# Kernel tuning notes

Hardware: AMD Instinct MI355X
Metric: run time of the kernel (lower is better)

Reference implementation:

```python
import jax, jax.numpy as jnp
import numpy as np

B, D, H, E, K = 16384, 4096, 2048, 64, 2
TEMPERATURE = 0.8  # training=True


def setup_inputs() -> dict:
    key = jax.random.key(0)
    k1, k2, k3 = jax.random.split(key, 3)
    x = jax.random.normal(k1, (B, D), dtype=jnp.float32)
    W1 = jax.random.normal(k2, (H, D), dtype=jnp.float32) * 0.02
    b1 = jnp.zeros((H,), dtype=jnp.float32)
    W2 = jax.random.normal(k3, (E, H), dtype=jnp.float32) * 0.02
    b2 = jnp.zeros((E,), dtype=jnp.float32)
    return {"x": x, "W1": W1, "b1": b1, "W2": W2, "b2": b2}


def reference(x, W1, b1, W2, b2):
    # router MLP: Linear(D->H) -> ReLU -> Linear(H->E)
    h = jax.nn.relu(jnp.einsum('bd,hd->bh', x, W1) + b1)
    router_logits = jnp.einsum('bh,eh->be', h, W2) + b2  # [B, E]

    # temperature-scaled softmax for routing
    routing_probs = jax.nn.softmax(router_logits / TEMPERATURE, axis=1)
    routing_weights, expert_indices = jax.lax.top_k(routing_probs, K)  # [B, K]
    routing_weights = routing_weights / routing_weights.sum(axis=1, keepdims=True)

    # entropy-based uncertainty uses UN-scaled logits
    full_probs = jax.nn.softmax(router_logits, axis=1)
    entropy = -jnp.sum(full_probs * jnp.log(full_probs + 1e-10), axis=1).mean()
    uncertainty = entropy / jnp.log(jnp.float32(E))
    return routing_weights, expert_indices, uncertainty
```

## Files before the change

### kernel.cpp

```cpp
#include <hip/hip_runtime.h>
#include <hip/hip_bf16.h>
#include <math.h>

#define B_ROWS 16384
#define D_DIM  4096
#define H_DIM  2048
#define E_DIM  64
#define TEMP   0.8f

typedef __bf16 bf16x8 __attribute__((ext_vector_type(8)));
typedef float  f32x4  __attribute__((ext_vector_type(4)));
typedef unsigned short ushort8 __attribute__((ext_vector_type(8)));

__device__ __forceinline__ unsigned short bf_rne(float f) {
  unsigned u = __float_as_uint(f);
  u += 0x7FFF + ((u >> 16) & 1);
  return (unsigned short)(u >> 16);
}

__device__ __forceinline__ void async_copy16(const void* g, void* l) {
  __builtin_amdgcn_global_load_lds(
      (const __attribute__((address_space(1))) void*)g,
      (__attribute__((address_space(3))) void*)l, 16, 0, 0);
}

__global__ __launch_bounds__(256) void split_kernel(
    const float* __restrict__ in, unsigned short* __restrict__ hi,
    unsigned short* __restrict__ lo) {
  const size_t i = ((size_t)blockIdx.x * 256 + threadIdx.x) * 8;
  float4 v0 = *(const float4*)(in + i);
  float4 v1 = *(const float4*)(in + i + 4);
  float f[8] = {v0.x, v0.y, v0.z, v0.w, v1.x, v1.y, v1.z, v1.w};
  ushort8 hv, lv;
#pragma unroll
  for (int j = 0; j < 8; ++j) {
    unsigned short h = bf_rne(f[j]);
    float fh = __uint_as_float(((unsigned)h) << 16);
    hv[j] = h;
    lv[j] = bf_rne(f[j] - fh);
  }
  *(ushort8*)(hi + i) = hv;
  *(ushort8*)(lo + i) = lv;
}

#define G_BM 256
#define G_BN 256
#define G_BK 32
#define G_NT (D_DIM / G_BK)

#define MFMA_TRIPLE(MIv, NIv, FAH, FAL, FBH, FBL)                               \
  _Pragma("unroll")                                                             \
  for (int mf = 0; mf < 4; ++mf) {                                              \
    _Pragma("unroll")                                                           \
    for (int nf = 0; nf < 2; ++nf) {                                            \
      f32x4 a = acc[MIv][mf][NIv][nf];                                          \
      a = __builtin_amdgcn_mfma_f32_16x16x32_bf16(FAH[mf], FBH[nf], a, 0, 0, 0);\
      a = __builtin_amdgcn_mfma_f32_16x16x32_bf16(FAL[mf], FBH[nf], a, 0, 0, 0);\
      a = __builtin_amdgcn_mfma_f32_16x16x32_bf16(FAH[mf], FBL[nf], a, 0, 0, 0);\
      acc[MIv][mf][NIv][nf] = a;                                                \
    }                                                                           \
  }

__global__ __launch_bounds__(512, 2) void gemm1_8ph_kernel(
    const unsigned short* __restrict__ xh, const unsigned short* __restrict__ xl,
    const unsigned short* __restrict__ w1h, const unsigned short* __restrict__ w1l,
    const float* __restrict__ b1,
    const unsigned short* __restrict__ w2h, const unsigned short* __restrict__ w2l,
    float* __restrict__ logitsP) {
  __shared__ unsigned short SMEM[65536];
  unsigned short* const LAh = SMEM;
  unsigned short* const LAl = SMEM + 16384;
  unsigned short* const LBh = SMEM + 32768;
  unsigned short* const LBl = SMEM + 49152;

  const int t    = threadIdx.x;
  const int lane = t & 63;
  const int w    = t >> 6;
  const int wm   = w >> 2;
  const int wn   = w & 3;

  const int wg   = blockIdx.x;
  const int xcd  = wg & 7;
  const int slot = wg >> 3;
  const int mt   = xcd * 8 + (slot >> 3);
  const int nt   = slot & 7;
  const int m0   = mt * G_BM;
  const int n0   = nt * G_BN;

  const int sr  = t >> 2;
  const int sc  = (t & 3) * 8;
  const int scs = sc ^ (((sr >> 1) & 3) << 3);
  const int t8  = t * 8;
  const unsigned short* gAh = xh  + (size_t)(m0 + sr) * D_DIM + scs;
  const unsigned short* gAl = xl  + (size_t)(m0 + sr) * D_DIM + scs;
  const unsigned short* gBh = w1h + (size_t)(n0 + sr) * D_DIM + scs;
  const unsigned short* gBl = w1l + (size_t)(n0 + sr) * D_DIM + scs;

  auto stageA = [&](int buf, int half, int kt) {
    const size_t go = (size_t)half * 128 * D_DIM + (size_t)kt * G_BK;
    const int lo = buf * 8192 + half * 4096 + t8;
    async_copy16(gAh + go, &LAh[lo]);
    async_copy16(gAl + go, &LAl[lo]);
  };
  auto stageB = [&](int buf, int half, int kt) {
    const size_t go = (size_t)half * 128 * D_DIM + (size_t)kt * G_BK;
    const int lo = buf * 8192 + half * 4096 + t8;
    async_copy16(gBh + go, &LBh[lo]);
    async_copy16(gBl + go, &LBl[lo]);
  };

  constexpr int SST[8] = {0,1,0,1,0,1,0,1};
  constexpr int SHF[8] = {1,1,0,0,1,1,0,0};
  constexpr int SBF[8] = {1,1,0,0,0,0,1,1};
  constexpr int STL[8] = {1,1,2,2,2,2,3,3};

  auto stagePhase = [&](int p, int i) {
    int tl = 2 * i + STL[p];
    if (tl > G_NT - 1) tl = G_NT - 1;
    if (SST[p] == 0) stageA(SBF[p], SHF[p], tl);
    else             stageB(SBF[p], SHF[p], tl);
  };

  const int fr = lane & 15;
  const int ko = (lane >> 4) * 8;
  const int fc = ko ^ (((fr >> 1) & 3) << 3);
  const int aO = (wm * 64 + fr) * 32 + fc;
  const int bO = (wn * 32 + fr) * 32 + fc;

  f32x4 acc[2][4][2][2];
#pragma unroll
  for (int a = 0; a < 2; ++a)
#pragma unroll
    for (int b = 0; b < 4; ++b)
#pragma unroll
      for (int c = 0; c < 2; ++c)
#pragma unroll
        for (int d = 0; d < 2; ++d) acc[a][b][c][d] = (f32x4)0.f;

  stageA(0, 0, 0); stageB(0, 0, 0);
  stageA(0, 1, 0); stageB(0, 1, 0);
  stageA(1, 0, 1); stageB(1, 0, 1);
  asm volatile("s_waitcnt vmcnt(4)" ::: "memory");
  __builtin_amdgcn_s_barrier();
  __builtin_amdgcn_sched_barrier(0);

  for (int i = 0; i < G_NT / 2; ++i) {
#pragma unroll
    for (int half = 0; half < 2; ++half) {
      const int base = half * 4;
      const int cb   = half * 8192;

      bf16x8 fah[4], fal[4];
      bf16x8 fbh0[2], fbl0[2];
      bf16x8 fbh1[2], fbl1[2];

#pragma unroll
      for (int mf = 0; mf < 4; ++mf) {
        fah[mf] = *(const bf16x8*)&LAh[cb + aO + mf * 512];
        fal[mf] = *(const bf16x8*)&LAl[cb + aO + mf * 512];
      }
#pragma unroll
      for (int nf = 0; nf < 2; ++nf) {
        fbh0[nf] = *(const bf16x8*)&LBh[cb + bO + nf * 512];
        fbl0[nf] = *(const bf16x8*)&LBl[cb + bO + nf * 512];
      }
      stagePhase(base + 0, i);
      __builtin_amdgcn_s_barrier();
      __builtin_amdgcn_sched_barrier(0);
      __builtin_amdgcn_s_setprio(1);
      MFMA_TRIPLE(0, 0, fah, fal, fbh0, fbl0)
      __builtin_amdgcn_s_setprio(0);
      __builtin_amdgcn_s_barrier();
      __builtin_amdgcn_sched_barrier(0);

#pragma unroll
      for (int nf = 0; nf < 2; ++nf) {
        fbh1[nf] = *(const bf16x8*)&LBh[cb + 4096 + bO + nf * 512];
        fbl1[nf] = *(const bf16x8*)&LBl[cb + 4096 + bO + nf * 512];
      }
      stagePhase(base + 1, i);
      __builtin_amdgcn_s_barrier();
      __builtin_amdgcn_sched_barrier(0);
      __builtin_amdgcn_s_setprio(1);
      MFMA_TRIPLE(0, 1, fah, fal, fbh1, fbl1)
      __builtin_amdgcn_s_setprio(0);
      __builtin_amdgcn_s_barrier();
      __builtin_amdgcn_sched_barrier(0);

#pragma unroll
      for (int mf = 0; mf < 4; ++mf) {
        fah[mf] = *(const bf16x8*)&LAh[cb + 4096 + aO + mf * 512];
        fal[mf] = *(const bf16x8*)&LAl[cb + 4096 + aO + mf * 512];
      }
      stagePhase(base + 2, i);
      __builtin_amdgcn_s_barrier();
      __builtin_amdgcn_sched_barrier(0);
      __builtin_amdgcn_s_setprio(1);
      MFMA_TRIPLE(1, 0, fah, fal, fbh0, fbl0)
      __builtin_amdgcn_s_setprio(0);
      __builtin_amdgcn_s_barrier();
      __builtin_amdgcn_sched_barrier(0);

      stagePhase(base + 3, i);
      __builtin_amdgcn_s_barrier();
      __builtin_amdgcn_sched_barrier(0);
      __builtin_amdgcn_s_setprio(1);
      MFMA_TRIPLE(1, 1, fah, fal, fbh1, fbl1)
      __builtin_amdgcn_s_setprio(0);
      asm volatile("s_waitcnt vmcnt(4)" ::: "memory");
      __builtin_amdgcn_s_barrier();
      __builtin_amdgcn_sched_barrier(0);
    }
  }
  asm volatile("s_waitcnt vmcnt(0)" ::: "memory");
  __syncthreads();

  unsigned short* const Hh = SMEM;
  unsigned short* const Hl = SMEM + 32768;

#pragma unroll
  for (int mi = 0; mi < 2; ++mi) {
#pragma unroll
    for (int ni = 0; ni < 2; ++ni)
#pragma unroll
      for (int nf = 0; nf < 2; ++nf) {
        const int colb = wn * 32 + ni * 128 + nf * 16 + fr;
        const float bias = b1[n0 + colb];
        const int u = colb >> 3, j = colb & 7;
#pragma unroll
        for (int mf = 0; mf < 4; ++mf) {
          const int rowb = wm * 64 + mf * 16 + (lane >> 4) * 4;
#pragma unroll
          for (int r = 0; r < 4; ++r) {
            const int rr = rowb + r;
            const float vv = fmaxf(acc[mi][mf][ni][nf][r] + bias, 0.f);
            const unsigned short hv = bf_rne(vv);
            const float fh = __uint_as_float(((unsigned)hv) << 16);
            const unsigned short lv = bf_rne(vv - fh);
            const int a = rr * 256 + ((u ^ (rr & 7)) << 3) + j;
            Hh[a] = hv;
            Hl[a] = lv;
          }
        }
      }
    __syncthreads();

    f32x4 lac[4];
#pragma unroll
    for (int nf = 0; nf < 4; ++nf) lac[nf] = (f32x4)0.f;

    const int arow = w * 16 + fr;
#pragma unroll
    for (int kf = 0; kf < 8; ++kf) {
      const int au = (kf * 4 + (lane >> 4)) ^ (arow & 7);
      bf16x8 ahi = *(const bf16x8*)&Hh[arow * 256 + au * 8];
      bf16x8 alo = *(const bf16x8*)&Hl[arow * 256 + au * 8];
#pragma unroll
      for (int nf = 0; nf < 4; ++nf) {
        const size_t boff = (size_t)(nf * 16 + fr) * H_DIM + n0 + kf * 32 + ko;
        bf16x8 bhi = *(const bf16x8*)(w2h + boff);
        bf16x8 blo = *(const bf16x8*)(w2l + boff);
        lac[nf] = __builtin_amdgcn_mfma_f32_16x16x32_bf16(ahi, bhi, lac[nf], 0, 0, 0);
        lac[nf] = __builtin_amdgcn_mfma_f32_16x16x32_bf16(alo, bhi, lac[nf], 0, 0, 0);
        lac[nf] = __builtin_amdgcn_mfma_f32_16x16x32_bf16(ahi, blo, lac[nf], 0, 0, 0);
      }
    }

    float* lpb = logitsP + (size_t)nt * ((size_t)B_ROWS * E_DIM);
#pragma unroll
    for (int nf = 0; nf < 4; ++nf) {
      const int e = nf * 16 + fr;
#pragma unroll
      for (int r = 0; r < 4; ++r) {
        const int grow = m0 + mi * 128 + w * 16 + (lane >> 4) * 4 + r;
        lpb[(size_t)grow * E_DIM + e] = lac[nf][r];
      }
    }
    __syncthreads();
  }
}

__global__ __launch_bounds__(256) void router_kernel(
    const float* __restrict__ lp, const float* __restrict__ b2,
    float* __restrict__ out, float* __restrict__ accum) {
  const int t = threadIdx.x;
  const size_t row = (size_t)blockIdx.x * 256 + t;
  const size_t PS = (size_t)B_ROWS * E_DIM;

  float lg[64];
#pragma unroll
  for (int e4 = 0; e4 < 16; ++e4) {
    float4 v = *(const float4*)(lp + row * E_DIM + e4 * 4);
    lg[e4 * 4 + 0] = v.x; lg[e4 * 4 + 1] = v.y;
    lg[e4 * 4 + 2] = v.z; lg[e4 * 4 + 3] = v.w;
  }
#pragma unroll
  for (int p = 1; p < 8; ++p) {
#pragma unroll
    for (int e4 = 0; e4 < 16; ++e4) {
      float4 v = *(const float4*)(lp + (size_t)p * PS + row * E_DIM + e4 * 4);
      lg[e4 * 4 + 0] += v.x; lg[e4 * 4 + 1] += v.y;
      lg[e4 * 4 + 2] += v.z; lg[e4 * 4 + 3] += v.w;
    }
  }
#pragma unroll
  for (int e = 0; e < E_DIM; ++e) lg[e] += b2[e];

  float l0 = lg[0]; int i0 = 0;
  float l1 = -INFINITY; int i1 = -1;
#pragma unroll
  for (int e = 1; e < E_DIM; ++e) {
    float v = lg[e];
    if (v > l0)      { l1 = l0; i1 = i0; l0 = v; i0 = e; }
    else if (v > l1) { l1 = v; i1 = e; }
  }

  const float eT = expf((l1 - l0) / TEMP);
  const float w0 = 1.f / (1.f + eT);
  const float w1 = eT / (1.f + eT);

  float Z = 0.f;
#pragma unroll
  for (int e = 0; e < E_DIM; ++e) Z += expf(lg[e] - l0);
  const float invZ = 1.f / Z;
  float ent = 0.f;
#pragma unroll
  for (int e = 0; e < E_DIM; ++e) {
    float p = expf(lg[e] - l0) * invZ;
    ent -= p * logf(p + 1e-10f);
  }

  out[row * 2 + 0] = w0;
  out[row * 2 + 1] = w1;
  out[(size_t)B_ROWS * 2 + row * 2 + 0] = (float)i0;
  out[(size_t)B_ROWS * 2 + row * 2 + 1] = (float)i1;

#pragma unroll
  for (int off = 32; off > 0; off >>= 1) ent += __shfl_down(ent, off);
  if ((t & 63) == 0) atomicAdd(accum, ent);
}

#define BM 128
#define BN 128
#define BKK 32

__global__ __launch_bounds__(256) void gemm1_fb_kernel(
    const float* __restrict__ x,
    const unsigned short* __restrict__ w1h,
    const unsigned short* __restrict__ w1l,
    const float* __restrict__ b1,
    unsigned short* __restrict__ hhp, unsigned short* __restrict__ hlp) {
  __shared__ unsigned short Ah[BM * BKK];
  __shared__ unsigned short Al[BM * BKK];
  __shared__ unsigned short Bh[BN * BKK];
  __shared__ unsigned short Bl[BN * BKK];

  const int t    = threadIdx.x;
  const int lane = t & 63;
  const int w    = t >> 6;
  const int wm   = w >> 1;
  const int wn   = w & 1;
  const int m0   = blockIdx.y * BM;
  const int n0   = blockIdx.x * BN;

  const int e0 = (w * 2 + 0) * 512 + lane * 8;
  const int e1 = (w * 2 + 1) * 512 + lane * 8;
  const int r0 = e0 >> 5, c0 = e0 & 31;
  const int r1 = e1 >> 5, c1 = e1 & 31;
  const unsigned short* bh_g0 = w1h + (size_t)(n0 + r0) * D_DIM + c0;
  const unsigned short* bh_g1 = w1h + (size_t)(n0 + r1) * D_DIM + c1;
  const unsigned short* bl_g0 = w1l + (size_t)(n0 + r0) * D_DIM + c0;
  const unsigned short* bl_g1 = w1l + (size_t)(n0 + r1) * D_DIM + c1;
  unsigned short* bh_l0 = &Bh[e0];
  unsigned short* bh_l1 = &Bh[e1];
  unsigned short* bl_l0 = &Bl[e0];
  unsigned short* bl_l1 = &Bl[e1];

  const int ar = t >> 1;
  const int ac = (t & 1) * 16;
  const float* xp = x + (size_t)(m0 + ar) * D_DIM + ac;
  unsigned short* ah_w = &Ah[ar * BKK + ac];
  unsigned short* al_w = &Al[ar * BKK + ac];

  const int koff = (lane >> 4) * 8;
  const unsigned short* a_rd[4];
  const unsigned short* b_rd[4];
#pragma unroll
  for (int f = 0; f < 4; ++f) {
    a_rd[f] = &Ah[(wm * 64 + f * 16 + (lane & 15)) * BKK + koff];
    b_rd[f] = &Bh[(wn * 64 + f * 16 + (lane & 15)) * BKK + koff];
  }
  const int lo_off_a = (int)(Al - Ah);
  const int lo_off_b = (int)(Bl - Bh);

  f32x4 acc[4][4];
#pragma unroll
  for (int i = 0; i < 4; ++i)
#pragma unroll
    for (int j = 0; j < 4; ++j) acc[i][j] = (f32x4)0.f;

  for (int k0 = 0; k0 < D_DIM; k0 += BKK) {
    async_copy16(bh_g0 + k0, bh_l0);
    async_copy16(bh_g1 + k0, bh_l1);
    async_copy16(bl_g0 + k0, bl_l0);
    async_copy16(bl_g1 + k0, bl_l1);

    float4 v[4];
#pragma unroll
    for (int j = 0; j < 4; ++j) v[j] = *(const float4*)(xp + k0 + j * 4);
    float f[16] = {v[0].x, v[0].y, v[0].z, v[0].w, v[1].x, v[1].y, v[1].z, v[1].w,
                   v[2].x, v[2].y, v[2].z, v[2].w, v[3].x, v[3].y, v[3].z, v[3].w};
    ushort8 hv0, hv1, lv0, lv1;
#pragma unroll
    for (int j = 0; j < 8; ++j) {
      unsigned short h = bf_rne(f[j]);
      float fh = __uint_as_float(((unsigned)h) << 16);
      hv0[j] = h;
      lv0[j] = bf_rne(f[j] - fh);
    }
#pragma unroll
    for (int j = 0; j < 8; ++j) {
      unsigned short h = bf_rne(f[8 + j]);
      float fh = __uint_as_float(((unsigned)h) << 16);
      hv1[j] = h;
      lv1[j] = bf_rne(f[8 + j] - fh);
    }
    *(ushort8*)(ah_w)     = hv0;
    *(ushort8*)(ah_w + 8) = hv1;
    *(ushort8*)(al_w)     = lv0;
    *(ushort8*)(al_w + 8) = lv1;

    __syncthreads();

    bf16x8 fa_h[4], fa_l[4], fb_h[4], fb_l[4];
#pragma unroll
    for (int ff = 0; ff < 4; ++ff) {
      fa_h[ff] = *(const bf16x8*)(a_rd[ff]);
      fa_l[ff] = *(const bf16x8*)(a_rd[ff] + lo_off_a);
      fb_h[ff] = *(const bf16x8*)(b_rd[ff]);
      fb_l[ff] = *(const bf16x8*)(b_rd[ff] + lo_off_b);
    }
#pragma unroll
    for (int i = 0; i < 4; ++i)
#pragma unroll
      for (int j = 0; j < 4; ++j) {
        acc[i][j] = __builtin_amdgcn_mfma_f32_16x16x32_bf16(fa_h[i], fb_h[j], acc[i][j], 0, 0, 0);
        acc[i][j] = __builtin_amdgcn_mfma_f32_16x16x32_bf16(fa_l[i], fb_h[j], acc[i][j], 0, 0, 0);
        acc[i][j] = __builtin_amdgcn_mfma_f32_16x16x32_bf16(fa_h[i], fb_l[j], acc[i][j], 0, 0, 0);
      }
    __syncthreads();
  }

#pragma unroll
  for (int fn = 0; fn < 4; ++fn) {
    const int n = n0 + wn * 64 + fn * 16 + (lane & 15);
    const float bias = b1[n];
#pragma unroll
    for (int fm = 0; fm < 4; ++fm) {
      const int mbase = m0 + wm * 64 + fm * 16 + (lane >> 4) * 4;
#pragma unroll
      for (int r = 0; r < 4; ++r) {
        const float vv = fmaxf(acc[fm][fn][r] + bias, 0.f);
        const unsigned short hv = bf_rne(vv);
        const float fh = __uint_as_float(((unsigned)hv) << 16);
        const unsigned short lv = bf_rne(vv - fh);
        hhp[(size_t)(mbase + r) * H_DIM + n] = hv;
        hlp[(size_t)(mbase + r) * H_DIM + n] = lv;
      }
    }
  }
}

#define F_BM 64
#define F_BK 64
#define F_NT (H_DIM / F_BK)

__global__ __launch_bounds__(256) void gemm2_router_kernel(
    const unsigned short* __restrict__ hhp,
    const unsigned short* __restrict__ hlp,
    const unsigned short* __restrict__ w2h,
    const unsigned short* __restrict__ w2l,
    const float* __restrict__ b2,
    float* __restrict__ out, float* __restrict__ accum) {
  __shared__ unsigned short Ahs[2 * 4096];
  __shared__ unsigned short Als[2 * 4096];
  __shared__ unsigned short Bhs[2 * 4096];
  __shared__ unsigned short Bls[2 * 4096];
  __shared__ float LG[F_BM][E_DIM + 1];

  const int t    = threadIdx.x;
  const int lane = t & 63;
  const int w    = t >> 6;
  const int m0   = blockIdx.x * F_BM;

  const int srow = w * 8 + (lane >> 3);
  const int scol = ((lane & 7) * 8) ^ (((lane >> 3) & 7) << 3);
  const int t8   = t * 8;
  const unsigned short* gAh = hhp + (size_t)(m0 + srow) * H_DIM + scol;
  const unsigned short* gAl = hlp + (size_t)(m0 + srow) * H_DIM + scol;
  const unsigned short* gBh = w2h + (size_t)srow * H_DIM + scol;
  const unsigned short* gBl = w2l + (size_t)srow * H_DIM + scol;

  auto stage2 = [&](int buf, int kt) {
    const size_t k0 = (size_t)kt * F_BK;
#pragma unroll
    for (int c = 0; c < 2; ++c) {
      const size_t go = k0 + (size_t)c * 32 * H_DIM;
      const int lo = buf * 4096 + c * 2048 + t8;
      async_copy16(gAh + go, &Ahs[lo]);
      async_copy16(gAl + go, &Als[lo]);
      async_copy16(gBh + go, &Bhs[lo]);
      async_copy16(gBl + go, &Bls[lo]);
    }
  };

  const int fr = lane & 15;
  const int ko = (lane >> 4) * 8;
  const int Ra = w * 16 + fr;
  int aoff[2], boff[2][4];
#pragma unroll
  for (int kk = 0; kk < 2; ++kk) {
    aoff[kk] = Ra * 64 + ((kk * 32 + ko) ^ ((Ra & 7) << 3));
#pragma unroll
    for (int f = 0; f < 4; ++f) {
      const int Rb = f * 16 + fr;
      boff[kk][f] = Rb * 64 + ((kk * 32 + ko) ^ ((Rb & 7) << 3));
    }
  }

  f32x4 acc[4];
#pragma unroll
  for (int f = 0; f < 4; ++f) acc[f] = (f32x4)0.f;

  stage2(0, 0);
  int buf = 0;
  for (int kt = 0; kt < F_NT; ++kt) {
    if (kt + 1 < F_NT) {
      stage2(buf ^ 1, kt + 1);
      asm volatile("s_waitcnt vmcnt(8)" ::: "memory");
    } else {
      asm volatile("s_waitcnt vmcnt(0)" ::: "memory");
    }
    __builtin_amdgcn_s_barrier();
    __builtin_amdgcn_sched_barrier(0);
    const int bo = buf * 4096;
#pragma unroll
    for (int kk = 0; kk < 2; ++kk) {
      bf16x8 fa_h = *(const bf16x8*)&Ahs[bo + aoff[kk]];
      bf16x8 fa_l = *(const bf16x8*)&Als[bo + aoff[kk]];
#pragma unroll
      for (int f = 0; f < 4; ++f) {
        bf16x8 fb_h = *(const bf16x8*)&Bhs[bo + boff[kk][f]];
        bf16x8 fb_l = *(const bf16x8*)&Bls[bo + boff[kk][f]];
        acc[f] = __builtin_amdgcn_mfma_f32_16x16x32_bf16(fa_h, fb_h, acc[f], 0, 0, 0);
        acc[f] = __builtin_amdgcn_mfma_f32_16x16x32_bf16(fa_l, fb_h, acc[f], 0, 0, 0);
        acc[f] = __builtin_amdgcn_mfma_f32_16x16x32_bf16(fa_h, fb_l, acc[f], 0, 0, 0);
      }
    }
    __builtin_amdgcn_s_barrier();
    __builtin_amdgcn_sched_barrier(0);
    buf ^= 1;
  }

#pragma unroll
  for (int f = 0; f < 4; ++f) {
    const int e = f * 16 + fr;
    const float bias = b2[e];
#pragma unroll
    for (int r = 0; r < 4; ++r) {
      const int ml = w * 16 + (lane >> 4) * 4 + r;
      LG[ml][e] = acc[f][r] + bias;
    }
  }
  __syncthreads();

  if (t < F_BM) {
    const int row = m0 + t;
    float l0 = LG[t][0]; int i0 = 0;
    float l1 = -INFINITY; int i1 = -1;
#pragma unroll
    for (int e = 1; e < E_DIM; ++e) {
      float v = LG[t][e];
      if (v > l0)      { l1 = l0; i1 = i0; l0 = v; i0 = e; }
      else if (v > l1) { l1 = v; i1 = e; }
    }

    const float eT = expf((l1 - l0) / TEMP);
    const float w0 = 1.f / (1.f + eT);
    const float w1 = eT / (1.f + eT);

    float Z = 0.f;
#pragma unroll
    for (int e = 0; e < E_DIM; ++e) Z += expf(LG[t][e] - l0);
    const float invZ = 1.f / Z;
    float ent = 0.f;
#pragma unroll
    for (int e = 0; e < E_DIM; ++e) {
      float p = expf(LG[t][e] - l0) * invZ;
      ent -= p * logf(p + 1e-10f);
    }

    out[(size_t)row * 2 + 0] = w0;
    out[(size_t)row * 2 + 1] = w1;
    out[(size_t)B_ROWS * 2 + (size_t)row * 2 + 0] = (float)i0;
    out[(size_t)B_ROWS * 2 + (size_t)row * 2 + 1] = (float)i1;

#pragma unroll
    for (int off = 32; off > 0; off >>= 1) ent += __shfl_down(ent, off);
    if (t == 0) atomicAdd(accum, ent);
  }
}

__global__ void zero_kernel(float* p) { p[0] = 0.f; }

__global__ void finalize_kernel(const float* __restrict__ accum,
                                float* __restrict__ out) {
  out[(size_t)B_ROWS * 4] = accum[0] / ((float)B_ROWS * logf((float)E_DIM));
}

extern "C" void kernel_launch(void* const* d_in, const int* in_sizes, int n_in,
                              void* d_out, int out_size, void* d_ws,
                              size_t ws_size, hipStream_t stream) {
  const float* x  = (const float*)d_in[0];
  const float* W1 = (const float*)d_in[1];
  const float* b1 = (const float*)d_in[2];
  const float* W2 = (const float*)d_in[3];
  const float* b2 = (const float*)d_in[4];
  float* out = (float*)d_out;

  const size_t SZ_W1 = (size_t)H_DIM * D_DIM;
  const size_t SZ_W2 = (size_t)E_DIM * H_DIM;
  const size_t SZ_H  = (size_t)B_ROWS * H_DIM;
  const size_t SZ_X  = (size_t)B_ROWS * D_DIM;

  unsigned short* w1h = (unsigned short*)d_ws;
  unsigned short* w1l = w1h + SZ_W1;
  unsigned short* w2h = w1l + SZ_W1;
  unsigned short* w2l = w2h + SZ_W2;
  unsigned short* hhp = w2l + SZ_W2;
  unsigned short* hlp = hhp + SZ_H;
  float* logitsP      = (float*)hhp;
  float* accum        = (float*)(hlp + SZ_H);
  unsigned short* xh  = (unsigned short*)(accum + 64);
  unsigned short* xl  = xh + SZ_X;
  const size_t need_bytes = (size_t)((char*)(xl + SZ_X) - (char*)d_ws);
  const bool fast = ws_size >= need_bytes;

  zero_kernel<<<1, 1, 0, stream>>>(accum);

  split_kernel<<<(int)(SZ_W1 / (256 * 8)), 256, 0, stream>>>(W1, w1h, w1l);
  split_kernel<<<(int)(SZ_W2 / (256 * 8)), 256, 0, stream>>>(W2, w2h, w2l);

  if (fast) {
    split_kernel<<<(int)(SZ_X / (256 * 8)), 256, 0, stream>>>(x, xh, xl);
    gemm1_8ph_kernel<<<512, 512, 0, stream>>>(xh, xl, w1h, w1l, b1,
                                              w2h, w2l, logitsP);
    router_kernel<<<B_ROWS / 256, 256, 0, stream>>>(logitsP, b2, out, accum);
  } else {
    dim3 g1f(H_DIM / BN, B_ROWS / BM);
    gemm1_fb_kernel<<<g1f, 256, 0, stream>>>(x, w1h, w1l, b1, hhp, hlp);
    gemm2_router_kernel<<<B_ROWS / F_BM, 256, 0, stream>>>(hhp, hlp, w2h, w2l,
                                                           b2, out, accum);
  }

  finalize_kernel<<<1, 1, 0, stream>>>(accum, out);
}
```

Baseline: 1.043 ms.

## Software-pipeline LDS fragment loads ahead of MFMA phases in gemm1

Restructures the 8-phase GEMM1 main loop so that LDS fragment reads for the next phase, including the next half's A0/B0 fragments, are issued before the current MFMA block rather than after a barrier. Separate fah0/fah1 register sets allow the loads to overlap with matrix-core work, hiding LDS latency. It also swaps launch_bounds min-blocks for an explicit waves_per_eu(2,2) attribute. The extra live fragment registers raise VGPR pressure and could cause spills. Reading the next half's buffer early relies on the moved vmcnt wait and barrier ordering being correct.

Result: slower. 1.481 ms (+41.9%).

```diff
diff --git a/kernel.cpp b/kernel.cpp
--- a/kernel.cpp
+++ b/kernel.cpp
@@ -61,7 +61,9 @@
     }                                                                           \
   }
 
-__global__ __launch_bounds__(512, 2) void gemm1_8ph_kernel(
+__global__ __launch_bounds__(512)
+__attribute__((amdgpu_waves_per_eu(2, 2)))
+void gemm1_8ph_kernel(
     const unsigned short* __restrict__ xh, const unsigned short* __restrict__ xl,
     const unsigned short* __restrict__ w1h, const unsigned short* __restrict__ w1l,
     const float* __restrict__ b1,
@@ -144,70 +146,81 @@
   __builtin_amdgcn_s_barrier();
   __builtin_amdgcn_sched_barrier(0);
 
+  bf16x8 fah0[4], fal0[4], fah1[4], fal1[4];
+  bf16x8 fbh0[2], fbl0[2], fbh1[2], fbl1[2];
+
+#pragma unroll
+  for (int mf = 0; mf < 4; ++mf) {
+    fah0[mf] = *(const bf16x8*)&LAh[aO + mf * 512];
+    fal0[mf] = *(const bf16x8*)&LAl[aO + mf * 512];
+  }
+#pragma unroll
+  for (int nf = 0; nf < 2; ++nf) {
+    fbh0[nf] = *(const bf16x8*)&LBh[bO + nf * 512];
+    fbl0[nf] = *(const bf16x8*)&LBl[bO + nf * 512];
+  }
+
   for (int i = 0; i < G_NT / 2; ++i) {
 #pragma unroll
     for (int half = 0; half < 2; ++half) {
       const int base = half * 4;
       const int cb   = half * 8192;
-
-      bf16x8 fah[4], fal[4];
-      bf16x8 fbh0[2], fbl0[2];
-      bf16x8 fbh1[2], fbl1[2];
-
-#pragma unroll
-      for (int mf = 0; mf < 4; ++mf) {
-        fah[mf] = *(const bf16x8*)&LAh[cb + aO + mf * 512];
-        fal[mf] = *(const bf16x8*)&LAl[cb + aO + mf * 512];
-      }
-#pragma unroll
-      for (int nf = 0; nf < 2; ++nf) {
-        fbh0[nf] = *(const bf16x8*)&LBh[cb + bO + nf * 512];
-        fbl0[nf] = *(const bf16x8*)&LBl[cb + bO + nf * 512];
-      }
+      const int cbn  = cb ^ 8192;
+
       stagePhase(base + 0, i);
       __builtin_amdgcn_s_barrier();
       __builtin_amdgcn_sched_barrier(0);
-      __builtin_amdgcn_s_setprio(1);
-      MFMA_TRIPLE(0, 0, fah, fal, fbh0, fbl0)
-      __builtin_amdgcn_s_setprio(0);
-      __builtin_amdgcn_s_barrier();
-      __builtin_amdgcn_sched_barrier(0);
-
 #pragma unroll
       for (int nf = 0; nf < 2; ++nf) {
         fbh1[nf] = *(const bf16x8*)&LBh[cb + 4096 + bO + nf * 512];
         fbl1[nf] = *(const bf16x8*)&LBl[cb + 4096 + bO + nf * 512];
       }
+      __builtin_amdgcn_s_setprio(1);
+      MFMA_TRIPLE(0, 0, fah0, fal0, fbh0, fbl0)
+      __builtin_amdgcn_s_setprio(0);
+      __builtin_amdgcn_s_barrier();
+      __builtin_amdgcn_sched_barrier(0);
+
       stagePhase(base + 1, i);
       __builtin_amdgcn_s_barrier();
       __builtin_amdgcn_sched_barrier(0);
+#pragma unroll
+      for (int mf = 0; mf < 4; ++mf) {
+        fah1[mf] = *(const bf16x8*)&LAh[cb + 4096 + aO + mf * 512];
+        fal1[mf] = *(const bf16x8*)&LAl[cb + 4096 + aO + mf * 512];
+      }
       __builtin_amdgcn_s_setprio(1);
-      MFMA_TRIPLE(0, 1, fah, fal, fbh1, fbl1)
+      MFMA_TRIPLE(0, 1, fah0, fal0, fbh1, fbl1)
       __builtin_amdgcn_s_setprio(0);
       __builtin_amdgcn_s_barrier();
       __builtin_amdgcn_sched_barrier(0);
 
+      stagePhase(base + 2, i);
+      __builtin_amdgcn_s_barrier();
+      __builtin_amdgcn_sched_barrier(0);
+      __builtin_amdgcn_s_setprio(1);
+      MFMA_TRIPLE(1, 0, fah1, fal1, fbh0, fbl0)
+      __builtin_amdgcn_s_setprio(0);
+      __builtin_amdgcn_s_barrier();
+      __builtin_amdgcn_sched_barrier(0);
+
+      stagePhase(base + 3, i);
+      __builtin_amdgcn_s_barrier();
+      __builtin_amdgcn_sched_barrier(0);
+      asm volatile("s_waitcnt vmcnt(4)" ::: "memory");
 #pragma unroll
       for (int mf = 0; mf < 4; ++mf) {
-        fah[mf] = *(const bf16x8*)&LAh[cb + 4096 + aO + mf * 512];
-        fal[mf] = *(const bf16x8*)&LAl[cb + 4096 + aO + mf * 512];
-      }
-      stagePhase(base + 2, i);
-      __builtin_amdgcn_s_barrier();
-      __builtin_amdgcn_sched_barrier(0);
+        fah0[mf] = *(const bf16x8*)&LAh[cbn + aO + mf * 512];
+        fal0[mf] = *(const bf16x8*)&LAl[cbn + aO + mf * 512];
+      }
+#pragma unroll
+      for (int nf = 0; nf < 2; ++nf) {
+        fbh0[nf] = *(const bf16x8*)&LBh[cbn + bO + nf * 512];
+        fbl0[nf] = *(const bf16x8*)&LBl[cbn + bO + nf * 512];
+      }
       __builtin_amdgcn_s_setprio(1);
-      MFMA_TRIPLE(1, 0, fah, fal, fbh0, fbl0)
+      MFMA_TRIPLE(1, 1, fah1, fal1, fbh1, fbl1)
       __builtin_amdgcn_s_setprio(0);
-      __builtin_amdgcn_s_barrier();
-      __builtin_amdgcn_sched_barrier(0);
-
-      stagePhase(base + 3, i);
-      __builtin_amdgcn_s_barrier();
-      __builtin_amdgcn_sched_barrier(0);
-      __builtin_amdgcn_s_setprio(1);
-      MFMA_TRIPLE(1, 1, fah, fal, fbh1, fbl1)
-      __builtin_amdgcn_s_setprio(0);
-      asm volatile("s_waitcnt vmcnt(4)" ::: "memory");
       __builtin_amdgcn_s_barrier();
       __builtin_amdgcn_sched_barrier(0);
     }
```
